# Performance work log

Measured on AMD Instinct MI355X. Metric: run time of the kernel, lower is better.

## Reference

```python
import jax, jax.numpy as jnp
import numpy as np
from math import sqrt

B = 16
SEQ = 2048          # tokens per sequence (equal-length jagged layout)
L = B * SEQ         # total tokens
D = 512             # embedding dim
P = 8192            # num_position_buckets
NTB = 2048          # num_time_buckets (ts table has NTB+1 rows)
TIME_BUCKET_INCREMENTS = 60.0
TIME_BUCKET_SCALE = 1.0
TIME_DELTA = 0.0
MAX_CONTEXTUAL_SEQ_LEN = 0


def setup_inputs() -> dict:
    key = jax.random.key(0)
    k_emb, k_pos, k_ts, k_time, k_tgt = jax.random.split(key, 5)
    seq_embeddings = jax.random.normal(k_emb, (L, D), dtype=jnp.float32)
    sp = sqrt(1.0 / P)
    pos_weight = jax.random.uniform(k_pos, (P, D), minval=-sp, maxval=sp, dtype=jnp.float32)
    st = sqrt(1.0 / NTB)
    ts_weight = jax.random.uniform(k_ts, (NTB + 1, D), minval=-st, maxval=st, dtype=jnp.float32)
    seq_timestamps = jnp.sort(jax.random.randint(k_time, (L,), 0, 1000000, dtype=jnp.int64) if jax.config.jax_enable_x64 else jax.random.randint(k_time, (L,), 0, 1000000).astype(jnp.int32))
    seq_lengths = jnp.full((B,), SEQ, dtype=jnp.int32)
    seq_offsets = jnp.arange(B + 1, dtype=jnp.int32) * SEQ
    num_targets = jax.random.randint(k_tgt, (B,), 0, 128).astype(jnp.int32)
    return {
        "max_seq_len": SEQ,
        "seq_lengths": seq_lengths,
        "seq_offsets": seq_offsets,
        "seq_embeddings": seq_embeddings,
        "num_targets": num_targets,
        "seq_timestamps": seq_timestamps,
        "pos_weight": pos_weight,
        "ts_weight": ts_weight,
    }


def reference(max_seq_len, seq_lengths, seq_offsets, seq_embeddings,
              num_targets, seq_timestamps, pos_weight, ts_weight):
    total_tokens, dim = seq_embeddings.shape
    batch_size = seq_lengths.shape[0]
    alpha = float(dim) ** 0.5

    # scale residual stream (done before the add in the time-encoding path)
    x = seq_embeddings * alpha

    lengths = seq_offsets[1:] - seq_offsets[:-1]            # [B]
    batch_ids = jnp.repeat(jnp.arange(batch_size, dtype=jnp.int32),
                           lengths, total_repeat_length=total_tokens)  # [L]
    row_ids = jnp.arange(total_tokens, dtype=jnp.int32)
    rel_pos = row_ids - seq_offsets[batch_ids].astype(jnp.int32)        # [L]

    # per-batch high index: seq_len - num_targets (interleave_targets=False)
    high_ind_pb = jnp.maximum(seq_lengths, 0) - jnp.maximum(num_targets, 0)
    high_ind_pb = jnp.maximum(high_ind_pb, 0)
    high_ind = high_ind_pb[batch_ids].astype(jnp.int32)                 # [L]

    max_pos_ind = pos_weight.shape[0]
    pos_ind = jnp.where(rel_pos < high_ind, rel_pos, high_ind)
    pos_ind = high_ind - pos_ind + MAX_CONTEXTUAL_SEQ_LEN
    pos_ind = jnp.minimum(pos_ind, max_pos_ind - 1)
    pos_ind = jnp.where(rel_pos < MAX_CONTEXTUAL_SEQ_LEN, rel_pos, pos_ind)
    pos_ind = jnp.clip(pos_ind, 0, max_pos_ind - 1)

    # timestamp bucket index (time_bucket_fn='sqrt')
    seq_end = seq_offsets[1:]
    query_time_pb = seq_timestamps[seq_end - 1]                         # [B]
    qt = query_time_pb[batch_ids].astype(jnp.float32)
    tt = seq_timestamps.astype(jnp.float32)
    dt = jnp.maximum(qt - tt + TIME_DELTA, 1e-6) / TIME_BUCKET_INCREMENTS
    dt = jnp.sqrt(dt) * TIME_BUCKET_SCALE
    ts_ind = dt.astype(jnp.int32)
    ts_ind = jnp.clip(ts_ind, 0, NTB)
    ts_ind = jnp.minimum(ts_ind, ts_weight.shape[0] - 1)

    # fused gather + add
    return x + (pos_weight[pos_ind] + ts_weight[ts_ind]).astype(x.dtype)
```

## Files before the change

kernel.cpp:

```cpp
#include <hip/hip_runtime.h>
#include <hip/hip_bf16.h>


typedef float f32x4 __attribute__((ext_vector_type(4)));

__global__ __launch_bounds__(256) void hstu_pos_enc_kernel(
    const f32x4* __restrict__ emb4,
    const f32x4* __restrict__ posw4,
    const f32x4* __restrict__ tsw4,
    const int*   __restrict__ seq_offsets,
    const int*   __restrict__ seq_lengths,
    const int*   __restrict__ num_targets,
    const int*   __restrict__ seq_ts,
    f32x4* __restrict__ out4,
    int L, int D4, int B, int P, int NTB, float alpha)
{
    const int row  = blockIdx.x * 4 + (threadIdx.x >> 6);
    const int lane = threadIdx.x & 63;
    if (row >= L) return;

    int b = 0;
    while (b + 1 < B && seq_offsets[b + 1] <= row) ++b;

    const int rel_pos = row - seq_offsets[b];

    int high_ind = max(seq_lengths[b], 0) - max(num_targets[b], 0);
    high_ind = max(high_ind, 0);

    int pos_ind = (rel_pos < high_ind) ? rel_pos : high_ind;
    pos_ind = high_ind - pos_ind;
    pos_ind = max(min(pos_ind, P - 1), 0);

    const float qt = (float)seq_ts[seq_offsets[b + 1] - 1];
    const float tt = (float)seq_ts[row];
    float dt = fmaxf(qt - tt, 1e-6f) * (1.0f / 60.0f);
    dt = sqrtf(dt);
    int ts_ind = (int)dt;
    ts_ind = max(min(ts_ind, NTB), 0);

    const long ebase = (long)row * D4;
    const long pbase = (long)pos_ind * D4;
    const long tbase = (long)ts_ind  * D4;

    if (D4 == 128) {
        const f32x4 e0 = __builtin_nontemporal_load(&emb4[ebase + lane]);
        const f32x4 e1 = __builtin_nontemporal_load(&emb4[ebase + lane + 64]);
        const f32x4 p0 = posw4[pbase + lane];
        const f32x4 p1 = posw4[pbase + lane + 64];
        const f32x4 t0 = tsw4[tbase + lane];
        const f32x4 t1 = tsw4[tbase + lane + 64];

        f32x4 o0 = e0 * alpha + (p0 + t0);
        f32x4 o1 = e1 * alpha + (p1 + t1);
        __builtin_nontemporal_store(o0, &out4[ebase + lane]);
        __builtin_nontemporal_store(o1, &out4[ebase + lane + 64]);
    } else {
        for (int s = lane; s < D4; s += 64) {
            const f32x4 e = __builtin_nontemporal_load(&emb4[ebase + s]);
            const f32x4 p = posw4[pbase + s];
            const f32x4 t = tsw4[tbase + s];
            f32x4 o = e * alpha + (p + t);
            __builtin_nontemporal_store(o, &out4[ebase + s]);
        }
    }
}

extern "C" void kernel_launch(void* const* d_in, const int* in_sizes, int n_in,
                              void* d_out, int out_size, void* d_ws, size_t ws_size,
                              hipStream_t stream) {
    const int*   seq_lengths = (const int*)d_in[1];
    const int*   seq_offsets = (const int*)d_in[2];
    const float* emb         = (const float*)d_in[3];
    const int*   num_targets = (const int*)d_in[4];
    const int*   seq_ts      = (const int*)d_in[5];
    const float* posw        = (const float*)d_in[6];
    const float* tsw         = (const float*)d_in[7];

    const int B   = in_sizes[1];
    const int L   = in_sizes[5];
    const int D   = in_sizes[3] / L;
    const int D4  = D / 4;
    const int P   = in_sizes[6] / D;
    const int NTB = in_sizes[7] / D - 1;
    const float alpha = sqrtf((float)D);

    const int rows_per_block = 4;
    const int grid = (L + rows_per_block - 1) / rows_per_block;

    hstu_pos_enc_kernel<<<grid, 256, 0, stream>>>(
        (const f32x4*)emb, (const f32x4*)posw, (const f32x4*)tsw,
        seq_offsets, seq_lengths, num_targets, seq_ts,
        (f32x4*)d_out, L, D4, B, P, NTB, alpha);
}
```

Baseline: 31.47 us.

## Process four rows per wavefront and find batch via ballot instead of linear search

Each wavefront now handles four consecutive rows, so one block covers 16 rows and the grid shrinks fourfold. Per-batch metadata is loaded once per lane and the batch id is found with a ballot/popcount, replacing the serial scan over seq_offsets, with values fetched by shuffles. All loads for the four rows are issued before any arithmetic to raise memory-level parallelism. This costs more registers per thread and leaves fewer blocks to spread across the GPU.

```diff
diff --git a/kernel.cpp b/kernel.cpp
--- a/kernel.cpp
+++ b/kernel.cpp
@@ -15,52 +15,102 @@
     f32x4* __restrict__ out4,
     int L, int D4, int B, int P, int NTB, float alpha)
 {
-    const int row  = blockIdx.x * 4 + (threadIdx.x >> 6);
+    const int wv   = threadIdx.x >> 6;
     const int lane = threadIdx.x & 63;
-    if (row >= L) return;
+    const int row0 = blockIdx.x * 16 + wv * 4;
+    if (row0 >= L) return;
 
-    int b = 0;
-    while (b + 1 < B && seq_offsets[b + 1] <= row) ++b;
+    const int off_l = seq_offsets[min(lane, B)];
+    const int len_l = seq_lengths[min(lane, B - 1)];
+    const int tgt_l = num_targets[min(lane, B - 1)];
+    const int qtidx = seq_offsets[min(lane + 1, B)] - 1;
+    const int qt_l  = seq_ts[max(qtidx, 0)];
+    const bool inr  = (lane >= 1) && (lane <= B);
 
-    const int rel_pos = row - seq_offsets[b];
+    int   rows[4];
+    int   pi[4], ti[4];
+    bool  has[4];
 
-    int high_ind = max(seq_lengths[b], 0) - max(num_targets[b], 0);
-    high_ind = max(high_ind, 0);
+    #pragma unroll
+    for (int r = 0; r < 4; ++r) {
+        rows[r] = row0 + r;
+        has[r]  = rows[r] < L;
+    }
+    const int rB = has[3] ? 3 : (has[2] ? 2 : (has[1] ? 1 : 0));
 
-    int pos_ind = (rel_pos < high_ind) ? rel_pos : high_ind;
-    pos_ind = high_ind - pos_ind;
-    pos_ind = max(min(pos_ind, P - 1), 0);
+    int tts[4];
+    #pragma unroll
+    for (int r = 0; r < 4; ++r) tts[r] = seq_ts[has[r] ? rows[r] : row0];
 
-    const float qt = (float)seq_ts[seq_offsets[b + 1] - 1];
-    const float tt = (float)seq_ts[row];
-    float dt = fmaxf(qt - tt, 1e-6f) * (1.0f / 60.0f);
-    dt = sqrtf(dt);
-    int ts_ind = (int)dt;
-    ts_ind = max(min(ts_ind, NTB), 0);
+    #pragma unroll
+    for (int r = 0; r < 4; ++r) {
+        const int row = has[r] ? rows[r] : row0;
+        int b;
+        if (B <= 63) {
+            b = __popcll(__ballot(inr && (row >= off_l)));
+        } else {
+            b = 0; while (b + 1 < B && seq_offsets[b + 1] <= row) ++b;
+        }
+        const int off_b = __shfl(off_l, min(b, 63));
+        const int len   = __shfl(len_l, min(b, 63));
+        const int tgt   = __shfl(tgt_l, min(b, 63));
+        const int qti   = __shfl(qt_l,  min(b, 63));
 
-    const long ebase = (long)row * D4;
-    const long pbase = (long)pos_ind * D4;
-    const long tbase = (long)ts_ind  * D4;
+        int high = max(len, 0) - max(tgt, 0);
+        high = max(high, 0);
+        int rel = row - off_b;
+        int p = (rel < high) ? rel : high;
+        p = high - p;
+        pi[r] = max(min(p, P - 1), 0);
+
+        float dtv = fmaxf((float)qti - (float)tts[r], 1e-6f) * (1.0f / 60.0f);
+        int t = (int)sqrtf(dtv);
+        ti[r] = max(min(t, NTB), 0);
+    }
 
     if (D4 == 128) {
-        const f32x4 e0 = __builtin_nontemporal_load(&emb4[ebase + lane]);
-        const f32x4 e1 = __builtin_nontemporal_load(&emb4[ebase + lane + 64]);
-        const f32x4 p0 = posw4[pbase + lane];
-        const f32x4 p1 = posw4[pbase + lane + 64];
-        const f32x4 t0 = tsw4[tbase + lane];
-        const f32x4 t1 = tsw4[tbase + lane + 64];
-
-        f32x4 o0 = e0 * alpha + (p0 + t0);
-        f32x4 o1 = e1 * alpha + (p1 + t1);
-        __builtin_nontemporal_store(o0, &out4[ebase + lane]);
-        __builtin_nontemporal_store(o1, &out4[ebase + lane + 64]);
+        f32x4 e[4][2], p[4][2], t[4][2];
+        #pragma unroll
+        for (int r = 0; r < 4; ++r) {
+            const int rr = has[r] ? r : rB;
+            const long eb = (long)rows[rr] * D4;
+            e[r][0] = __builtin_nontemporal_load(&emb4[eb + lane]);
+            e[r][1] = __builtin_nontemporal_load(&emb4[eb + lane + 64]);
+        }
+        #pragma unroll
+        for (int r = 0; r < 4; ++r) {
+            const int rr = has[r] ? r : rB;
+            const long pb = (long)pi[rr] * D4;
+            p[r][0] = posw4[pb + lane];
+            p[r][1] = posw4[pb + lane + 64];
+        }
+        #pragma unroll
+        for (int r = 0; r < 4; ++r) {
+            const int rr = has[r] ? r : rB;
+            const long tb = (long)ti[rr] * D4;
+            t[r][0] = tsw4[tb + lane];
+            t[r][1] = tsw4[tb + lane + 64];
+        }
+        #pragma unroll
+        for (int r = 0; r < 4; ++r) {
+            if (!has[r]) continue;
+            const long eb = (long)rows[r] * D4;
+            f32x4 o0 = e[r][0] * alpha + (p[r][0] + t[r][0]);
+            f32x4 o1 = e[r][1] * alpha + (p[r][1] + t[r][1]);
+            __builtin_nontemporal_store(o0, &out4[eb + lane]);
+            __builtin_nontemporal_store(o1, &out4[eb + lane + 64]);
+        }
     } else {
-        for (int s = lane; s < D4; s += 64) {
-            const f32x4 e = __builtin_nontemporal_load(&emb4[ebase + s]);
-            const f32x4 p = posw4[pbase + s];
-            const f32x4 t = tsw4[tbase + s];
-            f32x4 o = e * alpha + (p + t);
-            __builtin_nontemporal_store(o, &out4[ebase + s]);
+        for (int r = 0; r < 4; ++r) {
+            if (!has[r]) continue;
+            const long eb = (long)rows[r] * D4;
+            const long pb = (long)pi[r]  * D4;
+            const long tb = (long)ti[r]  * D4;
+            for (int s = lane; s < D4; s += 64) {
+                const f32x4 ev = __builtin_nontemporal_load(&emb4[eb + s]);
+                f32x4 o = ev * alpha + (posw4[pb + s] + tsw4[tb + s]);
+                __builtin_nontemporal_store(o, &out4[eb + s]);
+            }
         }
     }
 }
@@ -84,7 +134,7 @@
     const int NTB = in_sizes[7] / D - 1;
     const float alpha = sqrtf((float)D);
 
-    const int rows_per_block = 4;
+    const int rows_per_block = 16;
     const int grid = (L + rows_per_block - 1) / rows_per_block;
 
     hstu_pos_enc_kernel<<<grid, 256, 0, stream>>>(
```

Result: slower. 33.18 us (+5.4%).
